# Performance work log

Measured on AMD Instinct MI355X. Metric: run time of the kernel, lower is better.

## Reference

```python
import jax, jax.numpy as jnp
import numpy as np

DIM = 192
NUM_HEADS = 6
WS = (7, 7, 7)
N_TOK = WS[0] * WS[1] * WS[2]  # 343
TABLE_SIZE = (2 * WS[0] - 1) * (2 * WS[1] - 1) * (2 * WS[2] - 1)  # 2197


def _relative_position_index():
    # faithful replication of the torch buffer construction (incl. its strides)
    coords = np.stack(np.meshgrid(np.arange(WS[0]), np.arange(WS[1]), np.arange(WS[2]), indexing='ij'))
    flat = coords.reshape(3, -1)                     # [3, N]
    rel = flat[:, :, None] - flat[:, None, :]        # [3, N, N]
    rel = rel.transpose(1, 2, 0).astype(np.int64)    # [N, N, 3]
    rel[..., 0] += WS[0] - 1
    rel[..., 1] += WS[1] - 1
    rel[..., 2] += WS[2] - 1
    rel[..., 0] *= 3 * WS[1] - 1  # = 20 (source uses window_size[1] here)
    rel[..., 1] *= 2 * WS[1] - 1  # = 13
    return rel.sum(-1)            # [N, N]


def setup_inputs() -> dict:
    key = jax.random.key(0)
    ks = jax.random.split(key, 10)
    B_, nW = 256, 64
    x1 = jax.random.normal(ks[0], (B_, N_TOK, DIM), dtype=jnp.float32)
    x2 = jax.random.normal(ks[1], (B_, N_TOK, DIM), dtype=jnp.float32)
    mask = jax.random.normal(ks[2], (nW, N_TOK, N_TOK), dtype=jnp.float32)
    table = 0.02 * jax.random.normal(ks[3], (TABLE_SIZE, NUM_HEADS), dtype=jnp.float32)
    s = DIM ** -0.5
    q_w = s * jax.random.normal(ks[4], (DIM, DIM), dtype=jnp.float32)
    q_b = jnp.zeros((DIM,), jnp.float32)
    kv_w = s * jax.random.normal(ks[5], (2 * DIM, DIM), dtype=jnp.float32)
    kv_b = jnp.zeros((2 * DIM,), jnp.float32)
    proj_w = s * jax.random.normal(ks[6], (DIM, DIM), dtype=jnp.float32)
    proj_b = jnp.zeros((DIM,), jnp.float32)
    rel_idx = jnp.asarray(_relative_position_index(), dtype=jnp.int32)
    return {"x1": x1, "x2": x2, "mask": mask, "table": table,
            "q_w": q_w, "q_b": q_b, "kv_w": kv_w, "kv_b": kv_b,
            "proj_w": proj_w, "proj_b": proj_b, "rel_idx": rel_idx}


def reference(x1, x2, mask, table, q_w, q_b, kv_w, kv_b, proj_w, proj_b, rel_idx):
    B_, N, C = x1.shape
    H = NUM_HEADS
    hd = C // H
    scale = hd ** -0.5
    # q from x1, k/v from x2 (isfusion cross-attention path)
    q = (x1 @ q_w.T + q_b).reshape(B_, N, H, hd).transpose(0, 2, 1, 3) * scale  # [B,H,N,hd]
    kv = (x2 @ kv_w.T + kv_b).reshape(B_, N, 2, H, hd).transpose(2, 0, 3, 1, 4)  # [2,B,H,N,hd]
    k, v = kv[0], kv[1]
    attn = jnp.einsum('bhnd,bhmd->bhnm', q, k)  # [B,H,N,N]
    # relative position bias gather -> [H,N,N]
    bias = table[rel_idx.reshape(-1)].reshape(N, N, H).transpose(2, 0, 1)
    attn = attn + bias[None]
    # shifted-window mask add
    nW = mask.shape[0]
    attn = (attn.reshape(B_ // nW, nW, H, N, N) + mask[None, :, None]).reshape(B_, H, N, N)
    attn = jax.nn.softmax(attn, axis=-1)
    out = jnp.einsum('bhnm,bhmd->bnhd', attn, v).reshape(B_, N, C)
    return out @ proj_w.T + proj_b
```

## Files before the change

kernel.cpp:

```cpp
#include <hip/hip_runtime.h>

typedef __attribute__((ext_vector_type(8))) short short8;
typedef __attribute__((ext_vector_type(4))) float f32x4;
typedef __attribute__((ext_vector_type(16))) float f32x16;
typedef __attribute__((ext_vector_type(4))) unsigned short us4;
typedef __attribute__((ext_vector_type(2))) unsigned int u32x2;

#define NTOK 343
#define BMP 352
#define LOG2E 1.4426950408889634f
#define FPLANE 11264
#define WPITCH 200

#define OFF_QG   0u
#define OFF_KG   33718272u
#define OFF_VT   68321280u
#define OFF_AO   102924288u
#define OFF_WB   136642560u

__device__ __forceinline__ unsigned short f2bf(float f) {
  union { float f; unsigned u; } v; v.f = f;
  unsigned r = v.u + 0x7FFFu + ((v.u >> 16) & 1u);
  return (unsigned short)(r >> 16);
}

__device__ __forceinline__ float bf2f(unsigned short b) {
  union { unsigned u; float f; } v; v.u = ((unsigned)b) << 16;
  return v.f;
}

__device__ __forceinline__ short8 ld8(const unsigned short* p) {
  return *reinterpret_cast<const short8*>(p);
}

__device__ __forceinline__ float fexp2(float x) {
  float r; asm("v_exp_f32 %0, %1" : "=v"(r) : "v"(x)); return r;
}

__device__ __forceinline__ unsigned cvtpk(float a, float b) {
  unsigned r; asm("v_cvt_pk_bf16_f32 %0, %1, %2" : "=v"(r) : "v"(a), "v"(b)); return r;
}

__device__ __forceinline__ void plswap(unsigned &a, unsigned &b) {
  asm("v_permlane32_swap_b32 %0, %1" : "+v"(a), "+v"(b));
}

__device__ __forceinline__ f32x16 mfma32(short8 a, short8 b, f32x16 c) {
  return __builtin_amdgcn_mfma_f32_32x32x16_bf16(a, b, c, 0, 0, 0);
}

__device__ __forceinline__ f32x4 mfma16(short8 a, short8 b, f32x4 c) {
  return __builtin_amdgcn_mfma_f32_16x16x32_bf16(a, b, c, 0, 0, 0);
}

union frag_u { unsigned u[4]; short8 s8; };

__device__ __forceinline__ short8 cvt8f(const float* p) {
  f32x4 a = *reinterpret_cast<const f32x4*>(p);
  f32x4 b = *reinterpret_cast<const f32x4*>(p + 4);
  frag_u f;
  f.u[0] = cvtpk(a[0], a[1]); f.u[1] = cvtpk(a[2], a[3]);
  f.u[2] = cvtpk(b[0], b[1]); f.u[3] = cvtpk(b[2], b[3]);
  return f.s8;
}

__global__ __launch_bounds__(256) void precompute(
    const float* __restrict__ mask, const float* __restrict__ table,
    const int* __restrict__ rel_idx,
    const float* __restrict__ qw, const float* __restrict__ kvw, const float* __restrict__ pw,
    unsigned short* __restrict__ wq_bf, unsigned short* __restrict__ wkv_bf,
    unsigned short* __restrict__ wp_bf,
    unsigned short* __restrict__ bias_bf, unsigned short* __restrict__ mask_bf,
    unsigned short* __restrict__ v_frag)
{
  const int idx = blockIdx.x * 256 + threadIdx.x;
  if (idx < 36864) {
    const int wi = idx;
    const float* src; unsigned short* dst; int i;
    if (wi < 9216)       { src = qw;  dst = wq_bf;  i = wi; }
    else if (wi < 27648) { src = kvw; dst = wkv_bf; i = wi - 9216; }
    else                 { src = pw;  dst = wp_bf;  i = wi - 27648; }
    f32x4 v = *reinterpret_cast<const f32x4*>(src + i * 4);
    us4 o; o[0] = f2bf(v[0]); o[1] = f2bf(v[1]); o[2] = f2bf(v[2]); o[3] = f2bf(v[3]);
    *reinterpret_cast<us4*>(dst + i * 4) = o;
  } else if (idx < 1968640) {
    const int mi = idx - 36864;
    const int row = mi / 88, q = mi - row * 88;
    const int j0 = q * 4;
    unsigned short* dst = mask_bf + row * BMP + j0;
    if (q < 85) {
      const float* src = mask + row * NTOK + j0;
      us4 o; o[0] = f2bf(LOG2E * src[0]); o[1] = f2bf(LOG2E * src[1]);
      o[2] = f2bf(LOG2E * src[2]); o[3] = f2bf(LOG2E * src[3]);
      *reinterpret_cast<us4*>(dst) = o;
    } else {
      us4 o;
      #pragma unroll
      for (int i = 0; i < 4; ++i) {
        const int col = j0 + i;
        o[i] = (col < NTOK) ? f2bf(LOG2E * mask[row * NTOK + col]) : (unsigned short)0;
      }
      *reinterpret_cast<us4*>(dst) = o;
    }
  } else if (idx < 2086289) {
    const int i = idx - 1968640;
    const int ri = rel_idx[i] * 6;
    const int rrow = i / NTOK, j = i - rrow * NTOK;
    unsigned short* dst = bias_bf + rrow * BMP + j;
    #pragma unroll
    for (int h = 0; h < 6; ++h) dst[h * (NTOK * BMP)] = f2bf(LOG2E * table[ri + h]);
  } else if (idx < 2088347) {
    const int p = idx - 2086289;
    unsigned short* dst = bias_bf + p * BMP + NTOK;
    #pragma unroll
    for (int c = 0; c < 9; ++c) dst[c] = 0;
  } else if (idx < 2284955) {
    const int i = idx - 2088347;
    const int bh = i >> 7, c = i & 127;
    short8 z = (short8){0,0,0,0,0,0,0,0};
    *reinterpret_cast<short8*>(v_frag + bh * FPLANE + 10240 + c * 8) = z;
  }
}

__global__ __launch_bounds__(256) void proj(
    const float* __restrict__ x1f, const float* __restrict__ x2f,
    const unsigned short* __restrict__ wq_bf, const unsigned short* __restrict__ wkv_bf,
    const float* __restrict__ qb, const float* __restrict__ kvb,
    unsigned short* __restrict__ q_g, unsigned short* __restrict__ k_g,
    unsigned short* __restrict__ v_frag)
{
  __shared__ __align__(16) unsigned short wLds[192 * WPITCH];

  const int tid = threadIdx.x;
  const int wv = tid >> 6, lane = tid & 63, lg = lane >> 4, lr = lane & 15;
  const int path = blockIdx.y;
  const int b = blockIdx.x & 255, seg = blockIdx.x >> 8;
  const int n0 = seg * 128 + wv * 32;

  const float* X = (path == 0) ? x1f : x2f;
  const unsigned short* Wsrc = (path == 0) ? wq_bf : (path == 1 ? wkv_bf : wkv_bf + 36864);

  #pragma unroll
  for (int i = 0; i < 18; ++i) {
    const int c = i * 256 + tid;
    const int row = c / 24, c8 = c - row * 24;
    *reinterpret_cast<short8*>(&wLds[row * WPITCH + c8 * 8]) = ld8(Wsrc + row * 192 + c8 * 8);
  }
  __syncthreads();

  const int rowbase = b * NTOK;
  const int nA = n0 + lr, nB = n0 + 16 + lr;
  const float* xr0 = X + (rowbase + (nA < NTOK ? nA : NTOK - 1)) * 192 + lg * 8;
  const float* xr1 = X + (rowbase + (nB < NTOK ? nB : NTOK - 1)) * 192 + lg * 8;

  short8 ax[2][6];
  #pragma unroll
  for (int kk = 0; kk < 6; ++kk) {
    ax[0][kk] = cvt8f(xr0 + kk * 32);
    ax[1][kk] = cvt8f(xr1 + kk * 32);
  }

  f32x4 acc[2][12];
  #pragma unroll
  for (int i = 0; i < 2; ++i)
    #pragma unroll
    for (int j = 0; j < 12; ++j) acc[i][j] = (f32x4){0.f, 0.f, 0.f, 0.f};

  if (path < 2) {
    #pragma unroll
    for (int kk = 0; kk < 6; ++kk) {
      const int k0 = kk * 32 + lg * 8;
      #pragma unroll
      for (int ct = 0; ct < 12; ++ct) {
        const short8 wf = *reinterpret_cast<const short8*>(&wLds[(ct * 16 + lr) * WPITCH + k0]);
        acc[0][ct] = mfma16(wf, ax[0][kk], acc[0][ct]);
        acc[1][ct] = mfma16(wf, ax[1][kk], acc[1][ct]);
      }
    }
    if (path == 0) {
      const float qs = 0.17677669529663687f * LOG2E;
      #pragma unroll
      for (int tt = 0; tt < 2; ++tt) {
        const int n = n0 + tt * 16 + lr;
        if (n < NTOK) {
          unsigned short* ob = q_g + (b * 6 * NTOK + n) * 32;
          #pragma unroll
          for (int ct = 0; ct < 12; ++ct) {
            const f32x4 bb = *reinterpret_cast<const f32x4*>(qb + ct * 16 + lg * 4);
            u32x2 pk;
            pk[0] = cvtpk((acc[tt][ct][0] + bb[0]) * qs, (acc[tt][ct][1] + bb[1]) * qs);
            pk[1] = cvtpk((acc[tt][ct][2] + bb[2]) * qs, (acc[tt][ct][3] + bb[3]) * qs);
            *reinterpret_cast<u32x2*>(ob + (ct >> 1) * (NTOK * 32) + (ct & 1) * 16 + lg * 4) = pk;
          }
        }
      }
    } else {
      #pragma unroll
      for (int tt = 0; tt < 2; ++tt) {
        const int n = n0 + tt * 16 + lr;
        if (n < 352) {
          unsigned short* ob = k_g + b * 6 * FPLANE + (n >> 5) * 1024
                               + ((lg >> 1) * 32 + (n & 31)) * 8 + (lg & 1) * 4;
          #pragma unroll
          for (int ct = 0; ct < 12; ++ct) {
            const f32x4 bb = *reinterpret_cast<const f32x4*>(kvb + ct * 16 + lg * 4);
            u32x2 pk;
            pk[0] = cvtpk(acc[tt][ct][0] + bb[0], acc[tt][ct][1] + bb[1]);
            pk[1] = cvtpk(acc[tt][ct][2] + bb[2], acc[tt][ct][3] + bb[3]);
            *reinterpret_cast<u32x2*>(ob + (ct >> 1) * FPLANE + (ct & 1) * 512) = pk;
          }
        }
      }
    }
  } else {
    #pragma unroll
    for (int kk = 0; kk < 6; ++kk) {
      const int k0 = kk * 32 + lg * 8;
      #pragma unroll
      for (int ct = 0; ct < 12; ++ct) {
        const short8 wf = *reinterpret_cast<const short8*>(&wLds[(ct * 16 + lr) * WPITCH + k0]);
        acc[0][ct] = mfma16(ax[0][kk], wf, acc[0][ct]);
        acc[1][ct] = mfma16(ax[1][kk], wf, acc[1][ct]);
      }
    }
    float bs[12];
    #pragma unroll
    for (int ct = 0; ct < 12; ++ct) bs[ct] = kvb[192 + ct * 16 + lr];
    #pragma unroll
    for (int tt = 0; tt < 2; ++tt) {
      const int nb = n0 + tt * 16 + lg * 4;
      if (nb < 352) {
        unsigned short* vb = v_frag + b * 6 * FPLANE + (nb >> 5) * 1024
                             + ((nb >> 4) & 1) * 512 + ((nb >> 3) & 1) * 256 + (nb & 7);
        #pragma unroll
        for (int ct = 0; ct < 12; ++ct) {
          const int d = (ct & 1) * 16 + lr;
          u32x2 pk;
          pk[0] = cvtpk(acc[tt][ct][0] + bs[ct], acc[tt][ct][1] + bs[ct]);
          pk[1] = cvtpk(acc[tt][ct][2] + bs[ct], acc[tt][ct][3] + bs[ct]);
          *reinterpret_cast<u32x2*>(vb + (ct >> 1) * FPLANE + d * 8) = pk;
        }
      }
    }
  }
}

__global__ __launch_bounds__(384, 4) void attn(
    const unsigned short* __restrict__ q_g, const unsigned short* __restrict__ k_g,
    const unsigned short* __restrict__ v_frag, const unsigned short* __restrict__ bias_bf,
    const unsigned short* __restrict__ mask_bf, unsigned short* __restrict__ attn_out)
{
  __shared__ __align__(16) unsigned short kvlds[2][FPLANE];

  const int tid = threadIdx.x;
  const int wv = tid >> 6, lane = tid & 63;
  const int l31 = lane & 31, hi = lane >> 5;
  const int s0 = blockIdx.x;
  const int xcd = s0 & 7, ii = s0 >> 3;
  const int g = xcd * 48 + (ii >> 2), mem = ii & 3;
  const int h = g >> 6, w = g & 63;
  const int b = mem * 64 + w;
  const int bid = b * 6 + h;

  const unsigned short* qp = q_g + bid * (NTOK * 32);
  const unsigned short* kpf = k_g + bid * FPLANE;
  const unsigned short* vpf = v_frag + bid * FPLANE;
  const unsigned short* bias_h = bias_bf + h * (NTOK * BMP);
  const unsigned short* mask_w = mask_bf + w * (NTOK * BMP);

  #pragma unroll
  for (int j = 0; j < 4; ++j) {
    const int c = j * 384 + tid;
    if (c < 1408) {
      *reinterpret_cast<short8*>(&kvlds[0][c * 8]) = ld8(kpf + c * 8);
      *reinterpret_cast<short8*>(&kvlds[1][c * 8]) = ld8(vpf + c * 8);
    }
  }
  __syncthreads();

  for (int qt = wv; qt < 11; qt += 6) {
    const int qq = qt * 32 + l31;
    const int qrc = qq < NTOK ? qq : NTOK - 1;
    const short8 qf0 = ld8(qp + qrc * 32 + hi * 8);
    const short8 qf1 = ld8(qp + qrc * 32 + 16 + hi * 8);
    const unsigned short* bmb = bias_h + qrc * BMP + hi * 4;
    const unsigned short* bmm = mask_w + qrc * BMP + hi * 4;

    f32x16 O;
    #pragma unroll
    for (int r = 0; r < 16; ++r) O[r] = 0.f;
    f32x4 sacc = (f32x4){0.f, 0.f, 0.f, 0.f};

    us4 nb[4], nm[4];
    #pragma unroll
    for (int gg = 0; gg < 4; ++gg) {
      nb[gg] = *reinterpret_cast<const us4*>(bmb + gg * 8);
      nm[gg] = *reinterpret_cast<const us4*>(bmm + gg * 8);
    }

    #pragma unroll
    for (int kt = 0; kt < 11; ++kt) {
      us4 cb[4], cm[4];
      #pragma unroll
      for (int gg = 0; gg < 4; ++gg) { cb[gg] = nb[gg]; cm[gg] = nm[gg]; }
      if (kt < 10) {
        const int kn = (kt + 1) * 32;
        #pragma unroll
        for (int gg = 0; gg < 4; ++gg) {
          nb[gg] = *reinterpret_cast<const us4*>(bmb + kn + gg * 8);
          nm[gg] = *reinterpret_cast<const us4*>(bmm + kn + gg * 8);
        }
      }

      const short8 kf0 = ld8(&kvlds[0][kt * 1024 + lane * 8]);
      const short8 kf1 = ld8(&kvlds[0][kt * 1024 + 512 + lane * 8]);
      f32x16 sv;
      #pragma unroll
      for (int r = 0; r < 16; ++r) sv[r] = 0.f;
      __builtin_amdgcn_s_setprio(1);
      sv = mfma32(kf0, qf0, sv);
      sv = mfma32(kf1, qf1, sv);
      __builtin_amdgcn_s_setprio(0);

      float p[16];
      #pragma unroll
      for (int gg = 0; gg < 4; ++gg) {
        #pragma unroll
        for (int j = 0; j < 4; ++j) {
          float v = sv[gg * 4 + j] + (bf2f(cb[gg][j]) + bf2f(cm[gg][j]));
          if (kt == 10 && (gg * 8 + hi * 4 + j) >= 23) v = -3.0e38f;
          p[gg * 4 + j] = fexp2(v);
        }
      }
      #pragma unroll
      for (int j = 0; j < 4; ++j)
        sacc[j] += (p[j] + p[4 + j]) + (p[8 + j] + p[12 + j]);

      unsigned c01 = cvtpk(p[0], p[1]),   c23 = cvtpk(p[2], p[3]);
      unsigned c45 = cvtpk(p[4], p[5]),   c67 = cvtpk(p[6], p[7]);
      unsigned d01 = cvtpk(p[8], p[9]),   d23 = cvtpk(p[10], p[11]);
      unsigned d45 = cvtpk(p[12], p[13]), d67 = cvtpk(p[14], p[15]);
      plswap(c01, c45); plswap(c23, c67);
      plswap(d01, d45); plswap(d23, d67);
      frag_u P0, P1;
      P0.u[0] = c01; P0.u[1] = c23; P0.u[2] = c45; P0.u[3] = c67;
      P1.u[0] = d01; P1.u[1] = d23; P1.u[2] = d45; P1.u[3] = d67;

      const short8 vf0 = ld8(&kvlds[1][kt * 1024 + lane * 8]);
      const short8 vf1 = ld8(&kvlds[1][kt * 1024 + 512 + lane * 8]);
      __builtin_amdgcn_s_setprio(1);
      O = mfma32(vf0, P0.s8, O);
      O = mfma32(vf1, P1.s8, O);
      __builtin_amdgcn_s_setprio(0);
    }

    float sum = (sacc[0] + sacc[1]) + (sacc[2] + sacc[3]);
    sum += __shfl_xor(sum, 32);
    const float inv = 1.0f / sum;
    if (qq < NTOK) {
      unsigned short* op = attn_out + (b * NTOK + qq) * 192 + h * 32;
      #pragma unroll
      for (int gg = 0; gg < 4; ++gg) {
        us4 ov;
        #pragma unroll
        for (int j = 0; j < 4; ++j) ov[j] = f2bf(O[gg * 4 + j] * inv);
        *reinterpret_cast<us4*>(op + gg * 8 + hi * 4) = ov;
      }
    }
  }
}

__global__ __launch_bounds__(256) void proj_out(
    const unsigned short* __restrict__ a_in, const unsigned short* __restrict__ wp_bf,
    const float* __restrict__ pb, float* __restrict__ out)
{
  __shared__ __align__(16) unsigned short wLds[192 * WPITCH];

  const int tid = threadIdx.x;
  const int wv = tid >> 6, lane = tid & 63, lg = lane >> 4, lr = lane & 15;
  const int t0 = blockIdx.x * 128 + wv * 32;

  #pragma unroll
  for (int i = 0; i < 18; ++i) {
    const int c = i * 256 + tid;
    const int row = c / 24, c8 = c - row * 24;
    *reinterpret_cast<short8*>(&wLds[row * WPITCH + c8 * 8]) = ld8(wp_bf + row * 192 + c8 * 8);
  }
  __syncthreads();

  const unsigned short* xr0 = a_in + (t0 + lr) * 192 + lg * 8;
  const unsigned short* xr1 = xr0 + 16 * 192;

  short8 ax[2][6];
  #pragma unroll
  for (int kk = 0; kk < 6; ++kk) {
    ax[0][kk] = ld8(xr0 + kk * 32);
    ax[1][kk] = ld8(xr1 + kk * 32);
  }

  f32x4 acc[2][12];
  #pragma unroll
  for (int i = 0; i < 2; ++i)
    #pragma unroll
    for (int j = 0; j < 12; ++j) acc[i][j] = (f32x4){0.f, 0.f, 0.f, 0.f};

  #pragma unroll
  for (int kk = 0; kk < 6; ++kk) {
    const int k0 = kk * 32 + lg * 8;
    #pragma unroll
    for (int ct = 0; ct < 12; ++ct) {
      const short8 wf = *reinterpret_cast<const short8*>(&wLds[(ct * 16 + lr) * WPITCH + k0]);
      acc[0][ct] = mfma16(wf, ax[0][kk], acc[0][ct]);
      acc[1][ct] = mfma16(wf, ax[1][kk], acc[1][ct]);
    }
  }

  #pragma unroll
  for (int tt = 0; tt < 2; ++tt) {
    const int t = t0 + tt * 16 + lr;
    float* op = out + t * 192 + lg * 4;
    #pragma unroll
    for (int ct = 0; ct < 12; ++ct) {
      const f32x4 bb = *reinterpret_cast<const f32x4*>(pb + ct * 16 + lg * 4);
      f32x4 ov;
      #pragma unroll
      for (int r = 0; r < 4; ++r) ov[r] = acc[tt][ct][r] + bb[r];
      *reinterpret_cast<f32x4*>(op + ct * 16) = ov;
    }
  }
}

extern "C" void kernel_launch(void* const* d_in, const int* in_sizes, int n_in,
                              void* d_out, int out_size, void* d_ws, size_t ws_size,
                              hipStream_t stream) {
  const float* x1    = (const float*)d_in[0];
  const float* x2    = (const float*)d_in[1];
  const float* mask  = (const float*)d_in[2];
  const float* table = (const float*)d_in[3];
  const float* qw    = (const float*)d_in[4];
  const float* qb    = (const float*)d_in[5];
  const float* kvw   = (const float*)d_in[6];
  const float* kvb   = (const float*)d_in[7];
  const float* pw    = (const float*)d_in[8];
  const float* pb    = (const float*)d_in[9];
  const int* rel_idx = (const int*)d_in[10];

  char* ws = (char*)d_ws;
  char* outc = (char*)d_out;
  unsigned short* q_g     = (unsigned short*)(ws + OFF_QG);
  unsigned short* k_g     = (unsigned short*)(ws + OFF_KG);
  unsigned short* v_frag  = (unsigned short*)(ws + OFF_VT);
  unsigned short* a_o     = (unsigned short*)(ws + OFF_AO);
  unsigned short* wq_bf   = (unsigned short*)(ws + OFF_WB);
  unsigned short* wkv_bf  = wq_bf + 36864;
  unsigned short* wp_bf   = wkv_bf + 73728;
  unsigned short* bias_bf = (unsigned short*)(outc + 33718272);
  unsigned short* mask_bf = (unsigned short*)(outc + 35167104);

  hipLaunchKernelGGL(precompute, dim3(8926), dim3(256), 0, stream,
                     mask, table, rel_idx, qw, kvw, pw,
                     wq_bf, wkv_bf, wp_bf, bias_bf, mask_bf, v_frag);
  hipLaunchKernelGGL(proj, dim3(768, 3), dim3(256), 0, stream,
                     x1, x2, wq_bf, wkv_bf, qb, kvb, q_g, k_g, v_frag);
  hipLaunchKernelGGL(attn, dim3(1536), dim3(384), 0, stream,
                     q_g, k_g, v_frag, bias_bf, mask_bf, a_o);
  hipLaunchKernelGGL(proj_out, dim3(686), dim3(256), 0, stream,
                     a_o, wp_bf, pb, (float*)d_out);
}
```

Measured before the change: 223.1 us.

## Process two query tiles per wave in attention to reuse K/V fragments

The attention kernel drops from 6 to 4 waves per block. Each wave now handles query tiles wv and wv+4 together, sharing each K and V LDS fragment load across two MFMA chains, and waves 0-2 then take a third tile (wv+8). Bias and mask prefetch is moved after the softmax step, which is factored into a helper. This cuts LDS traffic per tile and gives the scheduler more independent MFMA work, at the cost of more registers (launch bounds 256,3) and an uneven tail where only three waves run the last tile.

```diff
diff --git a/kernel.cpp b/kernel.cpp
--- a/kernel.cpp
+++ b/kernel.cpp
@@ -62,6 +62,32 @@
   f.u[0] = cvtpk(a[0], a[1]); f.u[1] = cvtpk(a[2], a[3]);
   f.u[2] = cvtpk(b[0], b[1]); f.u[3] = cvtpk(b[2], b[3]);
   return f.s8;
+}
+
+__device__ __forceinline__ void smax(const f32x16& sv, const us4* cb, const us4* cm,
+                                     int kt, int hi, f32x4& sacc,
+                                     frag_u& P0, frag_u& P1) {
+  float p[16];
+  #pragma unroll
+  for (int gg = 0; gg < 4; ++gg) {
+    #pragma unroll
+    for (int j = 0; j < 4; ++j) {
+      float v = sv[gg * 4 + j] + (bf2f(cb[gg][j]) + bf2f(cm[gg][j]));
+      if (kt == 10 && (gg * 8 + hi * 4 + j) >= 23) v = -3.0e38f;
+      p[gg * 4 + j] = fexp2(v);
+    }
+  }
+  #pragma unroll
+  for (int j = 0; j < 4; ++j)
+    sacc[j] += (p[j] + p[4 + j]) + (p[8 + j] + p[12 + j]);
+  unsigned c01 = cvtpk(p[0], p[1]),   c23 = cvtpk(p[2], p[3]);
+  unsigned c45 = cvtpk(p[4], p[5]),   c67 = cvtpk(p[6], p[7]);
+  unsigned d01 = cvtpk(p[8], p[9]),   d23 = cvtpk(p[10], p[11]);
+  unsigned d45 = cvtpk(p[12], p[13]), d67 = cvtpk(p[14], p[15]);
+  plswap(c01, c45); plswap(c23, c67);
+  plswap(d01, d45); plswap(d23, d67);
+  P0.u[0] = c01; P0.u[1] = c23; P0.u[2] = c45; P0.u[3] = c67;
+  P1.u[0] = d01; P1.u[1] = d23; P1.u[2] = d45; P1.u[3] = d67;
 }
 
 __global__ __launch_bounds__(256) void precompute(
@@ -245,7 +271,7 @@
   }
 }
 
-__global__ __launch_bounds__(384, 4) void attn(
+__global__ __launch_bounds__(256, 3) void attn(
     const unsigned short* __restrict__ q_g, const unsigned short* __restrict__ k_g,
     const unsigned short* __restrict__ v_frag, const unsigned short* __restrict__ bias_bf,
     const unsigned short* __restrict__ mask_bf, unsigned short* __restrict__ attn_out)
@@ -269,8 +295,8 @@
   const unsigned short* mask_w = mask_bf + w * (NTOK * BMP);
 
   #pragma unroll
-  for (int j = 0; j < 4; ++j) {
-    const int c = j * 384 + tid;
+  for (int j = 0; j < 6; ++j) {
+    const int c = j * 256 + tid;
     if (c < 1408) {
       *reinterpret_cast<short8*>(&kvlds[0][c * 8]) = ld8(kpf + c * 8);
       *reinterpret_cast<short8*>(&kvlds[1][c * 8]) = ld8(vpf + c * 8);
@@ -278,7 +304,98 @@
   }
   __syncthreads();
 
-  for (int qt = wv; qt < 11; qt += 6) {
+  {
+    const int qqA = wv * 32 + l31;
+    const int qqB = (wv + 4) * 32 + l31;
+    const short8 qfA0 = ld8(qp + qqA * 32 + hi * 8);
+    const short8 qfA1 = ld8(qp + qqA * 32 + 16 + hi * 8);
+    const short8 qfB0 = ld8(qp + qqB * 32 + hi * 8);
+    const short8 qfB1 = ld8(qp + qqB * 32 + 16 + hi * 8);
+    const unsigned short* bmbA = bias_h + qqA * BMP + hi * 4;
+    const unsigned short* bmmA = mask_w + qqA * BMP + hi * 4;
+    const unsigned short* bmbB = bias_h + qqB * BMP + hi * 4;
+    const unsigned short* bmmB = mask_w + qqB * BMP + hi * 4;
+
+    f32x16 OA, OB;
+    #pragma unroll
+    for (int r = 0; r < 16; ++r) { OA[r] = 0.f; OB[r] = 0.f; }
+    f32x4 saccA = (f32x4){0.f, 0.f, 0.f, 0.f};
+    f32x4 saccB = (f32x4){0.f, 0.f, 0.f, 0.f};
+
+    us4 cbA[4], cmA[4], cbB[4], cmB[4];
+    #pragma unroll
+    for (int gg = 0; gg < 4; ++gg) {
+      cbA[gg] = *reinterpret_cast<const us4*>(bmbA + gg * 8);
+      cmA[gg] = *reinterpret_cast<const us4*>(bmmA + gg * 8);
+      cbB[gg] = *reinterpret_cast<const us4*>(bmbB + gg * 8);
+      cmB[gg] = *reinterpret_cast<const us4*>(bmmB + gg * 8);
+    }
+
+    #pragma unroll
+    for (int kt = 0; kt < 11; ++kt) {
+      const short8 kf0 = ld8(&kvlds[0][kt * 1024 + lane * 8]);
+      const short8 kf1 = ld8(&kvlds[0][kt * 1024 + 512 + lane * 8]);
+      f32x16 svA, svB;
+      #pragma unroll
+      for (int r = 0; r < 16; ++r) { svA[r] = 0.f; svB[r] = 0.f; }
+      __builtin_amdgcn_s_setprio(1);
+      svA = mfma32(kf0, qfA0, svA);
+      svA = mfma32(kf1, qfA1, svA);
+      svB = mfma32(kf0, qfB0, svB);
+      svB = mfma32(kf1, qfB1, svB);
+      __builtin_amdgcn_s_setprio(0);
+
+      frag_u PA0, PA1, PB0, PB1;
+      smax(svA, cbA, cmA, kt, hi, saccA, PA0, PA1);
+      smax(svB, cbB, cmB, kt, hi, saccB, PB0, PB1);
+
+      if (kt < 10) {
+        const int kn = (kt + 1) * 32;
+        #pragma unroll
+        for (int gg = 0; gg < 4; ++gg) {
+          cbA[gg] = *reinterpret_cast<const us4*>(bmbA + kn + gg * 8);
+          cmA[gg] = *reinterpret_cast<const us4*>(bmmA + kn + gg * 8);
+          cbB[gg] = *reinterpret_cast<const us4*>(bmbB + kn + gg * 8);
+          cmB[gg] = *reinterpret_cast<const us4*>(bmmB + kn + gg * 8);
+        }
+      }
+
+      const short8 vf0 = ld8(&kvlds[1][kt * 1024 + lane * 8]);
+      const short8 vf1 = ld8(&kvlds[1][kt * 1024 + 512 + lane * 8]);
+      __builtin_amdgcn_s_setprio(1);
+      OA = mfma32(vf0, PA0.s8, OA);
+      OA = mfma32(vf1, PA1.s8, OA);
+      OB = mfma32(vf0, PB0.s8, OB);
+      OB = mfma32(vf1, PB1.s8, OB);
+      __builtin_amdgcn_s_setprio(0);
+    }
+
+    float sumA = (saccA[0] + saccA[1]) + (saccA[2] + saccA[3]);
+    sumA += __shfl_xor(sumA, 32);
+    const float invA = 1.0f / sumA;
+    unsigned short* opA = attn_out + (b * NTOK + qqA) * 192 + h * 32;
+    #pragma unroll
+    for (int gg = 0; gg < 4; ++gg) {
+      us4 ov;
+      #pragma unroll
+      for (int j = 0; j < 4; ++j) ov[j] = f2bf(OA[gg * 4 + j] * invA);
+      *reinterpret_cast<us4*>(opA + gg * 8 + hi * 4) = ov;
+    }
+    float sumB = (saccB[0] + saccB[1]) + (saccB[2] + saccB[3]);
+    sumB += __shfl_xor(sumB, 32);
+    const float invB = 1.0f / sumB;
+    unsigned short* opB = attn_out + (b * NTOK + qqB) * 192 + h * 32;
+    #pragma unroll
+    for (int gg = 0; gg < 4; ++gg) {
+      us4 ov;
+      #pragma unroll
+      for (int j = 0; j < 4; ++j) ov[j] = f2bf(OB[gg * 4 + j] * invB);
+      *reinterpret_cast<us4*>(opB + gg * 8 + hi * 4) = ov;
+    }
+  }
+
+  if (wv + 8 < 11) {
+    const int qt = wv + 8;
     const int qq = qt * 32 + l31;
     const int qrc = qq < NTOK ? qq : NTOK - 1;
     const short8 qf0 = ld8(qp + qrc * 32 + hi * 8);
@@ -291,27 +408,15 @@
     for (int r = 0; r < 16; ++r) O[r] = 0.f;
     f32x4 sacc = (f32x4){0.f, 0.f, 0.f, 0.f};
 
-    us4 nb[4], nm[4];
+    us4 cb[4], cm[4];
     #pragma unroll
     for (int gg = 0; gg < 4; ++gg) {
-      nb[gg] = *reinterpret_cast<const us4*>(bmb + gg * 8);
-      nm[gg] = *reinterpret_cast<const us4*>(bmm + gg * 8);
+      cb[gg] = *reinterpret_cast<const us4*>(bmb + gg * 8);
+      cm[gg] = *reinterpret_cast<const us4*>(bmm + gg * 8);
     }
 
     #pragma unroll
     for (int kt = 0; kt < 11; ++kt) {
-      us4 cb[4], cm[4];
-      #pragma unroll
-      for (int gg = 0; gg < 4; ++gg) { cb[gg] = nb[gg]; cm[gg] = nm[gg]; }
-      if (kt < 10) {
-        const int kn = (kt + 1) * 32;
-        #pragma unroll
-        for (int gg = 0; gg < 4; ++gg) {
-          nb[gg] = *reinterpret_cast<const us4*>(bmb + kn + gg * 8);
-          nm[gg] = *reinterpret_cast<const us4*>(bmm + kn + gg * 8);
-        }
-      }
-
       const short8 kf0 = ld8(&kvlds[0][kt * 1024 + lane * 8]);
       const short8 kf1 = ld8(&kvlds[0][kt * 1024 + 512 + lane * 8]);
       f32x16 sv;
@@ -322,29 +427,17 @@
       sv = mfma32(kf1, qf1, sv);
       __builtin_amdgcn_s_setprio(0);
 
-      float p[16];
-      #pragma unroll
-      for (int gg = 0; gg < 4; ++gg) {
+      frag_u P0, P1;
+      smax(sv, cb, cm, kt, hi, sacc, P0, P1);
+
+      if (kt < 10) {
+        const int kn = (kt + 1) * 32;
         #pragma unroll
-        for (int j = 0; j < 4; ++j) {
-          float v = sv[gg * 4 + j] + (bf2f(cb[gg][j]) + bf2f(cm[gg][j]));
-          if (kt == 10 && (gg * 8 + hi * 4 + j) >= 23) v = -3.0e38f;
-          p[gg * 4 + j] = fexp2(v);
+        for (int gg = 0; gg < 4; ++gg) {
+          cb[gg] = *reinterpret_cast<const us4*>(bmb + kn + gg * 8);
+          cm[gg] = *reinterpret_cast<const us4*>(bmm + kn + gg * 8);
         }
       }
-      #pragma unroll
-      for (int j = 0; j < 4; ++j)
-        sacc[j] += (p[j] + p[4 + j]) + (p[8 + j] + p[12 + j]);
-
-      unsigned c01 = cvtpk(p[0], p[1]),   c23 = cvtpk(p[2], p[3]);
-      unsigned c45 = cvtpk(p[4], p[5]),   c67 = cvtpk(p[6], p[7]);
-      unsigned d01 = cvtpk(p[8], p[9]),   d23 = cvtpk(p[10], p[11]);
-      unsigned d45 = cvtpk(p[12], p[13]), d67 = cvtpk(p[14], p[15]);
-      plswap(c01, c45); plswap(c23, c67);
-      plswap(d01, d45); plswap(d23, d67);
-      frag_u P0, P1;
-      P0.u[0] = c01; P0.u[1] = c23; P0.u[2] = c45; P0.u[3] = c67;
-      P1.u[0] = d01; P1.u[1] = d23; P1.u[2] = d45; P1.u[3] = d67;
 
       const short8 vf0 = ld8(&kvlds[1][kt * 1024 + lane * 8]);
       const short8 vf1 = ld8(&kvlds[1][kt * 1024 + 512 + lane * 8]);
@@ -462,7 +555,7 @@
                      wq_bf, wkv_bf, wp_bf, bias_bf, mask_bf, v_frag);
   hipLaunchKernelGGL(proj, dim3(768, 3), dim3(256), 0, stream,
                      x1, x2, wq_bf, wkv_bf, qb, kvb, q_g, k_g, v_frag);
-  hipLaunchKernelGGL(attn, dim3(1536), dim3(384), 0, stream,
+  hipLaunchKernelGGL(attn, dim3(1536), dim3(256), 0, stream,
                      q_g, k_g, v_frag, bias_bf, mask_bf, a_o);
   hipLaunchKernelGGL(proj_out, dim3(686), dim3(256), 0, stream,
                      a_o, wp_bf, pb, (float*)d_out);
```

Result: slower. 411.4 us (+84.4%).
